# Optimization experiments

Measured on AMD Instinct MI355X. Metric: run time of the kernel, lower is better.

## Reference

```python
import jax, jax.numpy as jnp
import numpy as np

VALUE_SCALE = 0.1  # paper: values ~ N(0, (0.1*std)^2); weights are unit-std here


def setup_inputs() -> dict:
    key = jax.random.key(0)
    k1, k2, k3, k4 = jax.random.split(key, 4)
    O, I = 4096, 4096
    n_flip = 1_000_000
    x = jax.random.normal(k1, (256, I), dtype=jnp.float32)
    weight = jax.random.normal(k2, (O, I), dtype=jnp.float32)
    prune_mask = jax.random.uniform(k3, (O, I)) < 0.6
    weight = jnp.where(prune_mask, 0.0, weight)
    flip_idx = jax.random.randint(k4, (n_flip,), 0, O * I, dtype=jnp.int64)
    values = jax.random.normal(jax.random.fold_in(key, 7), (n_flip,), dtype=jnp.float32)
    return {"x": x, "weight": weight, "flip_idx": flip_idx, "values": values}


def reference(x, weight, flip_idx, values):
    # 'restore' mode: scatter small random values into pruned weight positions
    # (single fused scatter instead of a python loop of scalar writes),
    # then run the wrapped model's forward (Linear without bias).
    O, I = weight.shape
    w_flat = weight.reshape(-1)
    w_mod = w_flat.at[flip_idx].set(values * VALUE_SCALE).reshape(O, I)
    # y = x @ W^T  -- [B, I] x [O, I] -> [B, O]
    return jnp.einsum('bi,oi->bo', x, w_mod)
```

## Files before the change

### kernel.cpp

```cpp
#include <hip/hip_runtime.h>
#include <hip/hip_bf16.h>
#include <stdint.h>
#include <stddef.h>

#define BATCH 256
#define OC 4096
#define IC 4096
#define VALUE_SCALE 0.1f

#define BN 64
#define BK 32
#define KS 8
#define KPER (IC / KS)
#define NT (KPER / BK)
#define YSZ (BATCH * OC)

typedef float f32x4 __attribute__((ext_vector_type(4)));
typedef int   i32x4 __attribute__((ext_vector_type(4)));
typedef short bf16x8 __attribute__((ext_vector_type(8)));

__device__ __forceinline__ short f2bf(float f) {
    return (short)__bfloat16_as_ushort(__float2bfloat16(f));
}

__device__ __forceinline__ void barrier_nodrain() {
    asm volatile("s_waitcnt lgkmcnt(0)" ::: "memory");
    __builtin_amdgcn_sched_barrier(0);
    __builtin_amdgcn_s_barrier();
    __builtin_amdgcn_sched_barrier(0);
}

__global__ void scatter_k(float* __restrict__ w, const int* __restrict__ idx,
                          const float* __restrict__ val, int n) {
    int i = (blockIdx.x * blockDim.x + threadIdx.x) * 4;
    if (i + 4 <= n) {
        i32x4 id = *(const i32x4*)(idx + i);
        f32x4 v  = *(const f32x4*)(val + i);
        w[id[0]] = v[0] * VALUE_SCALE;
        w[id[1]] = v[1] * VALUE_SCALE;
        w[id[2]] = v[2] * VALUE_SCALE;
        w[id[3]] = v[3] * VALUE_SCALE;
    } else {
        for (int j = i; j < n; ++j) w[idx[j]] = val[j] * VALUE_SCALE;
    }
}

__global__ __launch_bounds__(512, 4) void gemm_k(const float* __restrict__ x,
                                                 const float* __restrict__ w,
                                                 float* __restrict__ part,
                                                 float* __restrict__ y) {
    const int tid  = threadIdx.x;
    const int lane = tid & 63;
    const int wv   = tid >> 6;
    const int bid  = blockIdx.x;
    const int ks   = bid & 7;
    const int bn   = bid >> 3;
    const int k0   = ks * KPER;
    const int nc0  = bn * BN;

    __shared__ __align__(16) short At[2][BATCH * BK];
    __shared__ __align__(16) short Bt[2][BN * BK];

    f32x4 acc[2][4];
#pragma unroll
    for (int m = 0; m < 2; ++m)
#pragma unroll
        for (int n = 0; n < 4; ++n) acc[m][n] = (f32x4)0.0f;

    const int arow = tid >> 1, ah = tid & 1;
    const int brow = tid >> 2, bq = tid & 3;

    f32x4 ra0[4], rb0[2], ra1[4], rb1[2];

    auto load_regs = [&](int t, f32x4* ra, f32x4* rb) {
        const float* s = x + (size_t)arow * IC + k0 + t * BK + ah * 16;
        ra[0] = *(const f32x4*)s;
        ra[1] = *(const f32x4*)(s + 4);
        ra[2] = *(const f32x4*)(s + 8);
        ra[3] = *(const f32x4*)(s + 12);
        if (tid < 256) {
            const float* sb = w + (size_t)(nc0 + brow) * IC + k0 + t * BK + bq * 8;
            rb[0] = *(const f32x4*)sb;
            rb[1] = *(const f32x4*)(sb + 4);
        }
    };

    auto write_lds = [&](int buf, const f32x4* ra, const f32x4* rb) {
        const int swa = (arow >> 1) & 3;
        bf16x8 v0, v1;
#pragma unroll
        for (int q = 0; q < 4; ++q) {
            v0[q] = f2bf(ra[0][q]); v0[q + 4] = f2bf(ra[1][q]);
            v1[q] = f2bf(ra[2][q]); v1[q + 4] = f2bf(ra[3][q]);
        }
        *(bf16x8*)&At[buf][arow * BK + ((2 * ah)     ^ swa) * 8] = v0;
        *(bf16x8*)&At[buf][arow * BK + ((2 * ah + 1) ^ swa) * 8] = v1;
        if (tid < 256) {
            bf16x8 vb;
#pragma unroll
            for (int q = 0; q < 4; ++q) { vb[q] = f2bf(rb[0][q]); vb[q + 4] = f2bf(rb[1][q]); }
            *(bf16x8*)&Bt[buf][brow * BK + (bq ^ ((brow >> 1) & 3)) * 8] = vb;
        }
    };

    auto compute = [&](int buf) {
        const int fr = lane & 15, cs = lane >> 4;
        bf16x8 a[2], b[4];
#pragma unroll
        for (int m = 0; m < 2; ++m) {
            int row = wv * 32 + m * 16 + fr;
            a[m] = *(const bf16x8*)&At[buf][row * BK + ((cs ^ ((row >> 1) & 3))) * 8];
        }
#pragma unroll
        for (int n = 0; n < 4; ++n) {
            int row = n * 16 + fr;
            b[n] = *(const bf16x8*)&Bt[buf][row * BK + ((cs ^ ((row >> 1) & 3))) * 8];
        }
#pragma unroll
        for (int n = 0; n < 4; ++n)
#pragma unroll
            for (int m = 0; m < 2; ++m)
                acc[m][n] = __builtin_amdgcn_mfma_f32_16x16x32_bf16(a[m], b[n], acc[m][n], 0, 0, 0);
    };

    load_regs(0, ra0, rb0);
    write_lds(0, ra0, rb0);
    load_regs(1, ra1, rb1);
    barrier_nodrain();

#pragma unroll 1
    for (int tt = 0; tt < NT / 2; ++tt) {
        const int t0 = 2 * tt, t1 = 2 * tt + 1;
        if (t0 + 2 < NT) load_regs(t0 + 2, ra0, rb0);
        compute(0);
        barrier_nodrain();
        write_lds(1, ra1, rb1);
        barrier_nodrain();
        if (t1 + 2 < NT) load_regs(t1 + 2, ra1, rb1);
        compute(1);
        barrier_nodrain();
        if (t0 + 2 < NT) {
            write_lds(0, ra0, rb0);
            barrier_nodrain();
        }
    }

    if (part) {
        float* dst = part + (size_t)ks * YSZ;
#pragma unroll
        for (int m = 0; m < 2; ++m) {
            int r0 = wv * 32 + m * 16 + (lane >> 4) * 4;
#pragma unroll
            for (int n = 0; n < 4; ++n) {
                int c = nc0 + n * 16 + (lane & 15);
#pragma unroll
                for (int rr = 0; rr < 4; ++rr)
                    dst[(size_t)(r0 + rr) * OC + c] = acc[m][n][rr];
            }
        }
    } else {
#pragma unroll
        for (int m = 0; m < 2; ++m) {
            int r0 = wv * 32 + m * 16 + (lane >> 4) * 4;
#pragma unroll
            for (int n = 0; n < 4; ++n) {
                int c = nc0 + n * 16 + (lane & 15);
#pragma unroll
                for (int rr = 0; rr < 4; ++rr)
                    atomicAdd(&y[(size_t)(r0 + rr) * OC + c], acc[m][n][rr]);
            }
        }
    }
}

__global__ void reduce_k(const float* __restrict__ part, float* __restrict__ y) {
    int i = (blockIdx.x * blockDim.x + threadIdx.x) * 4;
    f32x4 s = *(const f32x4*)(part + i);
#pragma unroll
    for (int p = 1; p < KS; ++p) s += *(const f32x4*)(part + (size_t)p * YSZ + i);
    *(f32x4*)(y + i) = s;
}

extern "C" void kernel_launch(void* const* d_in, const int* in_sizes, int n_in,
                              void* d_out, int out_size, void* d_ws, size_t ws_size,
                              hipStream_t stream) {
    const float* x  = (const float*)d_in[0];
    float*       w  = (float*)d_in[1];
    const int*   fi = (const int*)d_in[2];
    const float* fv = (const float*)d_in[3];
    float*       y  = (float*)d_out;
    const int nflip = in_sizes[2];

    const bool use_ws = ws_size >= (size_t)KS * YSZ * sizeof(float);
    float* part = use_ws ? (float*)d_ws : nullptr;

    if (!use_ws) hipMemsetAsync(d_out, 0, (size_t)out_size * sizeof(float), stream);
    scatter_k<<<dim3((nflip + 1023) / 1024), dim3(256), 0, stream>>>(w, fi, fv, nflip);
    gemm_k<<<dim3((OC / BN) * KS), dim3(512), 0, stream>>>(x, w, part, y);
    if (use_ws)
        reduce_k<<<dim3(YSZ / (4 * 256)), dim3(256), 0, stream>>>(part, y);
}
```

Baseline: 148.4 us.

## Pre-convert activations to swizzled bf16 tiles in workspace before GEMM

Adds a prep kernel that converts x to bf16 once and stores it pre-tiled and pre-swizzled in the workspace, so GEMM blocks read bf16 tiles directly and copy them to LDS without conversion. Previously every one of the 64 column blocks re-read fp32 x and converted it, which doubled the A-side traffic and added conversion ALU work in the inner loop. The cost is an extra kernel launch, a larger workspace requirement, and a naive fallback path when the workspace is too small.

```diff
diff --git a/kernel.cpp b/kernel.cpp
--- a/kernel.cpp
+++ b/kernel.cpp
@@ -14,6 +14,9 @@
 #define KPER (IC / KS)
 #define NT (KPER / BK)
 #define YSZ (BATCH * OC)
+#define TILE_SHORTS (BATCH * BK)
+#define PART_BYTES ((size_t)KS * YSZ * sizeof(float))
+#define AP_BYTES   ((size_t)(IC / BK) * TILE_SHORTS * sizeof(short))
 
 typedef float f32x4 __attribute__((ext_vector_type(4)));
 typedef int   i32x4 __attribute__((ext_vector_type(4)));
@@ -45,20 +48,36 @@
     }
 }
 
-__global__ __launch_bounds__(512, 4) void gemm_k(const float* __restrict__ x,
+__global__ void prep_k(const float* __restrict__ x, short* __restrict__ ap) {
+    const int i = blockIdx.x * 256 + threadIdx.x;
+    const int r = i >> 9;
+    const int k = (i & 511) * 8;
+    const int tg = k >> 5;
+    const int q  = (k >> 3) & 3;
+    const float* s = x + (size_t)r * IC + k;
+    f32x4 lo = *(const f32x4*)s;
+    f32x4 hi = *(const f32x4*)(s + 4);
+    bf16x8 v;
+#pragma unroll
+    for (int j = 0; j < 4; ++j) { v[j] = f2bf(lo[j]); v[j + 4] = f2bf(hi[j]); }
+    *(bf16x8*)&ap[(size_t)tg * TILE_SHORTS + r * BK + ((q ^ ((r >> 1) & 3)) * 8)] = v;
+}
+
+struct Bank { bf16x8 a0, a1; f32x4 b0, b1; };
+
+__global__ __launch_bounds__(512, 4) void gemm_k(const short* __restrict__ ap,
                                                  const float* __restrict__ w,
-                                                 float* __restrict__ part,
-                                                 float* __restrict__ y) {
+                                                 float* __restrict__ part) {
     const int tid  = threadIdx.x;
     const int lane = tid & 63;
     const int wv   = tid >> 6;
     const int bid  = blockIdx.x;
     const int ks   = bid & 7;
     const int bn   = bid >> 3;
+    const int nc0  = bn * BN;
     const int k0   = ks * KPER;
-    const int nc0  = bn * BN;
-
-    __shared__ __align__(16) short At[2][BATCH * BK];
+
+    __shared__ __align__(16) short At[2][TILE_SHORTS];
     __shared__ __align__(16) short Bt[2][BN * BK];
 
     f32x4 acc[2][4];
@@ -67,38 +86,28 @@
 #pragma unroll
         for (int n = 0; n < 4; ++n) acc[m][n] = (f32x4)0.0f;
 
-    const int arow = tid >> 1, ah = tid & 1;
     const int brow = tid >> 2, bq = tid & 3;
 
-    f32x4 ra0[4], rb0[2], ra1[4], rb1[2];
-
-    auto load_regs = [&](int t, f32x4* ra, f32x4* rb) {
-        const float* s = x + (size_t)arow * IC + k0 + t * BK + ah * 16;
-        ra[0] = *(const f32x4*)s;
-        ra[1] = *(const f32x4*)(s + 4);
-        ra[2] = *(const f32x4*)(s + 8);
-        ra[3] = *(const f32x4*)(s + 12);
+    Bank bk0, bk1;
+
+    auto load_regs = [&](int t, Bank& b) {
+        const short* s = ap + (size_t)(ks * NT + t) * TILE_SHORTS;
+        b.a0 = *(const bf16x8*)(s + tid * 8);
+        b.a1 = *(const bf16x8*)(s + 4096 + tid * 8);
         if (tid < 256) {
             const float* sb = w + (size_t)(nc0 + brow) * IC + k0 + t * BK + bq * 8;
-            rb[0] = *(const f32x4*)sb;
-            rb[1] = *(const f32x4*)(sb + 4);
+            b.b0 = *(const f32x4*)sb;
+            b.b1 = *(const f32x4*)(sb + 4);
         }
     };
 
-    auto write_lds = [&](int buf, const f32x4* ra, const f32x4* rb) {
-        const int swa = (arow >> 1) & 3;
-        bf16x8 v0, v1;
-#pragma unroll
-        for (int q = 0; q < 4; ++q) {
-            v0[q] = f2bf(ra[0][q]); v0[q + 4] = f2bf(ra[1][q]);
-            v1[q] = f2bf(ra[2][q]); v1[q + 4] = f2bf(ra[3][q]);
-        }
-        *(bf16x8*)&At[buf][arow * BK + ((2 * ah)     ^ swa) * 8] = v0;
-        *(bf16x8*)&At[buf][arow * BK + ((2 * ah + 1) ^ swa) * 8] = v1;
+    auto write_lds = [&](int buf, const Bank& b) {
+        *(bf16x8*)&At[buf][tid * 8]        = b.a0;
+        *(bf16x8*)&At[buf][4096 + tid * 8] = b.a1;
         if (tid < 256) {
             bf16x8 vb;
 #pragma unroll
-            for (int q = 0; q < 4; ++q) { vb[q] = f2bf(rb[0][q]); vb[q + 4] = f2bf(rb[1][q]); }
+            for (int q = 0; q < 4; ++q) { vb[q] = f2bf(b.b0[q]); vb[q + 4] = f2bf(b.b1[q]); }
             *(bf16x8*)&Bt[buf][brow * BK + (bq ^ ((brow >> 1) & 3)) * 8] = vb;
         }
     };
@@ -123,52 +132,38 @@
                 acc[m][n] = __builtin_amdgcn_mfma_f32_16x16x32_bf16(a[m], b[n], acc[m][n], 0, 0, 0);
     };
 
-    load_regs(0, ra0, rb0);
-    write_lds(0, ra0, rb0);
-    load_regs(1, ra1, rb1);
+    load_regs(0, bk0);
+    write_lds(0, bk0);
+    load_regs(1, bk1);
     barrier_nodrain();
 
 #pragma unroll 1
     for (int tt = 0; tt < NT / 2; ++tt) {
         const int t0 = 2 * tt, t1 = 2 * tt + 1;
-        if (t0 + 2 < NT) load_regs(t0 + 2, ra0, rb0);
+        if (t0 + 2 < NT) load_regs(t0 + 2, bk0);
         compute(0);
         barrier_nodrain();
-        write_lds(1, ra1, rb1);
+        write_lds(1, bk1);
         barrier_nodrain();
-        if (t1 + 2 < NT) load_regs(t1 + 2, ra1, rb1);
+        if (t1 + 2 < NT) load_regs(t1 + 2, bk1);
         compute(1);
         barrier_nodrain();
         if (t0 + 2 < NT) {
-            write_lds(0, ra0, rb0);
+            write_lds(0, bk0);
             barrier_nodrain();
         }
     }
 
-    if (part) {
-        float* dst = part + (size_t)ks * YSZ;
-#pragma unroll
-        for (int m = 0; m < 2; ++m) {
-            int r0 = wv * 32 + m * 16 + (lane >> 4) * 4;
-#pragma unroll
-            for (int n = 0; n < 4; ++n) {
-                int c = nc0 + n * 16 + (lane & 15);
-#pragma unroll
-                for (int rr = 0; rr < 4; ++rr)
-                    dst[(size_t)(r0 + rr) * OC + c] = acc[m][n][rr];
-            }
-        }
-    } else {
-#pragma unroll
-        for (int m = 0; m < 2; ++m) {
-            int r0 = wv * 32 + m * 16 + (lane >> 4) * 4;
-#pragma unroll
-            for (int n = 0; n < 4; ++n) {
-                int c = nc0 + n * 16 + (lane & 15);
-#pragma unroll
-                for (int rr = 0; rr < 4; ++rr)
-                    atomicAdd(&y[(size_t)(r0 + rr) * OC + c], acc[m][n][rr]);
-            }
+    float* dst = part + (size_t)ks * YSZ;
+#pragma unroll
+    for (int m = 0; m < 2; ++m) {
+        int r0 = wv * 32 + m * 16 + (lane >> 4) * 4;
+#pragma unroll
+        for (int n = 0; n < 4; ++n) {
+            int c = nc0 + n * 16 + (lane & 15);
+#pragma unroll
+            for (int rr = 0; rr < 4; ++rr)
+                dst[(size_t)(r0 + rr) * OC + c] = acc[m][n][rr];
         }
     }
 }
@@ -179,6 +174,18 @@
 #pragma unroll
     for (int p = 1; p < KS; ++p) s += *(const f32x4*)(part + (size_t)p * YSZ + i);
     *(f32x4*)(y + i) = s;
+}
+
+__global__ void naive_k(const float* __restrict__ x, const float* __restrict__ w,
+                        float* __restrict__ y) {
+    const int o = blockIdx.x;
+    const int b = threadIdx.x;
+    const float* xr = x + (size_t)b * IC;
+    const float* wr = w + (size_t)o * IC;
+    float s = 0.f;
+#pragma unroll 4
+    for (int k = 0; k < IC; ++k) s += xr[k] * wr[k];
+    y[(size_t)b * OC + o] = s;
 }
 
 extern "C" void kernel_launch(void* const* d_in, const int* in_sizes, int n_in,
@@ -191,12 +198,17 @@
     float*       y  = (float*)d_out;
     const int nflip = in_sizes[2];
 
-    const bool use_ws = ws_size >= (size_t)KS * YSZ * sizeof(float);
-    float* part = use_ws ? (float*)d_ws : nullptr;
-
-    if (!use_ws) hipMemsetAsync(d_out, 0, (size_t)out_size * sizeof(float), stream);
-    scatter_k<<<dim3((nflip + 1023) / 1024), dim3(256), 0, stream>>>(w, fi, fv, nflip);
-    gemm_k<<<dim3((OC / BN) * KS), dim3(512), 0, stream>>>(x, w, part, y);
-    if (use_ws)
+    const bool use_ws = ws_size >= PART_BYTES + AP_BYTES;
+
+    if (use_ws) {
+        float* part = (float*)d_ws;
+        short* ap   = (short*)((char*)d_ws + PART_BYTES);
+        prep_k<<<dim3(512), dim3(256), 0, stream>>>(x, ap);
+        scatter_k<<<dim3((nflip + 1023) / 1024), dim3(256), 0, stream>>>(w, fi, fv, nflip);
+        gemm_k<<<dim3((OC / BN) * KS), dim3(512), 0, stream>>>(ap, w, part);
         reduce_k<<<dim3(YSZ / (4 * 256)), dim3(256), 0, stream>>>(part, y);
-}
+    } else {
+        scatter_k<<<dim3((nflip + 1023) / 1024), dim3(256), 0, stream>>>(w, fi, fv, nflip);
+        naive_k<<<dim3(OC), dim3(BATCH), 0, stream>>>(x, w, y);
+    }
+}
```

New measurement: 139.9 us. 1.06x faster.
